# Performance work log

Measured on AMD Instinct MI355X. Metric: run time of the kernel, lower is better.

## Reference

```python
import jax, jax.numpy as jnp
import numpy as np

SCALE = 1.0


def _chamfer_pair(a, b):
    # a: [N,3], b: [M,3] -> (dist1 [N], dist2 [M]) squared NN distances
    # ||a-b||^2 = ||a||^2 + ||b||^2 - 2 a.b
    aa = jnp.sum(a * a, axis=-1)            # [N]
    bb = jnp.sum(b * b, axis=-1)            # [M]
    ab = jnp.einsum('nd,md->nm', a, b)      # [N,M]
    d = aa[:, None] + bb[None, :] - 2.0 * ab
    d = jnp.maximum(d, 0.0)
    return jnp.min(d, axis=1), jnp.min(d, axis=0)


def reference(p1, p2):
    # p1, p2: [B, N, 3]; scale applied before distance, matching the torch module
    a = p1 * SCALE
    b = p2 * SCALE
    dist1, dist2 = jax.vmap(_chamfer_pair)(a, b)  # [B,N], [B,M]
    # per-sample loss = mean(dist1) + mean(dist2); total averaged over batch
    per_sample = jnp.mean(dist1, axis=1) + jnp.mean(dist2, axis=1)  # [B]
    return jnp.mean(per_sample).reshape(1)


def setup_inputs() -> dict:
    key = jax.random.key(0)
    k1, k2 = jax.random.split(key)
    B, N, M = 4, 8192, 8192
    p1 = jax.random.normal(k1, (B, N, 3), dtype=jnp.float32)
    p2 = jax.random.normal(k2, (B, M, 3), dtype=jnp.float32)
    return {"p1": p1, "p2": p2}
```

## Files before the change

kernel.cpp:

```cpp
#include <hip/hip_runtime.h>
#include <math.h>

#define BATCH   4
#define NPTS    8192
#define THREADS 256
#define QPT     4
#define QPB     (THREADS * QPT)
#define QTILES  (NPTS / QPB)

static constexpr float SCALE = 1.0f;


template<int TCH>
__global__ __launch_bounds__(THREADS, 8)
void chamfer_min_kernel(const float* __restrict__ p1,
                        const float* __restrict__ p2,
                        float* __restrict__ pm)
{
    constexpr int CHUNK = NPTS / TCH;
    __shared__ float4 lds4[CHUNK];

    const int bid = blockIdx.x;
    const int c   = bid % TCH;
    const int qt  = (bid / TCH) % QTILES;
    const int b   = (bid / (TCH * QTILES)) % BATCH;
    const int dir = bid / (TCH * QTILES * BATCH);

    const float* qptr = (dir == 0 ? p1 : p2) + (size_t)b * NPTS * 3;
    const float* tptr = (dir == 0 ? p2 : p1) + (size_t)b * NPTS * 3;

    const float* tsrc = tptr + (size_t)c * CHUNK * 3;
    for (int i = threadIdx.x; i < CHUNK; i += THREADS) {
        const float x = tsrc[3 * i + 0] * SCALE;
        const float y = tsrc[3 * i + 1] * SCALE;
        const float z = tsrc[3 * i + 2] * SCALE;
        const float bb = fmaf(z, z, fmaf(y, y, x * x));
        lds4[i] = make_float4(-2.0f * x, -2.0f * y, -2.0f * z, bb);
    }

    const int t  = threadIdx.x;
    const int q0 = qt * QPB + t;
    float qx[QPT], qy[QPT], qz[QPT], qmin[QPT];
    #pragma unroll
    for (int k = 0; k < QPT; ++k) {
        const int q = q0 + k * THREADS;
        qx[k] = qptr[q * 3 + 0] * SCALE;
        qy[k] = qptr[q * 3 + 1] * SCALE;
        qz[k] = qptr[q * 3 + 2] * SCALE;
        qmin[k] = 3.0e38f;
    }

    __syncthreads();

    for (int j = 0; j < CHUNK; j += 8) {
        #pragma unroll
        for (int i = 0; i < 8; i += 2) {
            const float4 t0 = lds4[j + i];
            const float4 t1 = lds4[j + i + 1];
            #pragma unroll
            for (int k = 0; k < QPT; ++k) {
                float s0 = fmaf(qx[k], t0.x, t0.w);
                s0 = fmaf(qy[k], t0.y, s0);
                s0 = fmaf(qz[k], t0.z, s0);
                float s1 = fmaf(qx[k], t1.x, t1.w);
                s1 = fmaf(qy[k], t1.y, s1);
                s1 = fmaf(qz[k], t1.z, s1);
                qmin[k] = fminf(qmin[k], fminf(s0, s1));
            }
        }
    }

    #pragma unroll
    for (int k = 0; k < QPT; ++k) {
        const float aa = fmaf(qz[k], qz[k], fmaf(qy[k], qy[k], qx[k] * qx[k]));
        const int q = q0 + k * THREADS;
        pm[((size_t)(dir * BATCH + b) * NPTS + q) * TCH + c] = qmin[k] + aa;
    }
}

template<int TCH>
__global__ __launch_bounds__(512)
void chamfer_reduce_kernel(const float* __restrict__ pm,
                           float* __restrict__ bsum)
{
    const int idx = blockIdx.x * 512 + threadIdx.x;
    const float4* p4 = reinterpret_cast<const float4*>(pm + (size_t)idx * TCH);
    float m = 3.0e38f;
    #pragma unroll
    for (int i = 0; i < TCH / 4; ++i) {
        const float4 u = p4[i];
        m = fminf(m, fminf(fminf(u.x, u.y), fminf(u.z, u.w)));
    }
    m = fmaxf(m, 0.0f);

    #pragma unroll
    for (int o = 32; o > 0; o >>= 1) m += __shfl_down(m, o, 64);

    __shared__ float red[8];
    const int wave = threadIdx.x >> 6;
    const int lane = threadIdx.x & 63;
    if (lane == 0) red[wave] = m;
    __syncthreads();
    if (threadIdx.x == 0) {
        float s = 0.0f;
        #pragma unroll
        for (int w = 0; w < 8; ++w) s += red[w];
        bsum[blockIdx.x] = s;
    }
}

__global__ __launch_bounds__(64)
void chamfer_final_kernel(const float* __restrict__ bsum,
                          float* __restrict__ out)
{
    const int t = threadIdx.x;
    float s0 = bsum[t];
    float s1 = bsum[64 + t];
    #pragma unroll
    for (int o = 32; o > 0; o >>= 1) {
        s0 += __shfl_down(s0, o, 64);
        s1 += __shfl_down(s1, o, 64);
    }
    if (t == 0) {
        out[0] = s0 / (float)(BATCH * NPTS) + s1 / (float)(BATCH * NPTS);
    }
}

template<int TCH>
static void launch_all(const float* p1, const float* p2, float* out,
                       void* d_ws, hipStream_t stream)
{
    float* pm   = (float*)d_ws;
    float* bsum = pm + (size_t)2 * BATCH * NPTS * TCH;

    chamfer_min_kernel<TCH><<<2 * BATCH * QTILES * TCH, THREADS, 0, stream>>>(p1, p2, pm);
    chamfer_reduce_kernel<TCH><<<128, 512, 0, stream>>>(pm, bsum);
    chamfer_final_kernel<<<1, 64, 0, stream>>>(bsum, out);
}

extern "C" void kernel_launch(void* const* d_in, const int* in_sizes, int n_in,
                              void* d_out, int out_size, void* d_ws, size_t ws_size,
                              hipStream_t stream) {
    const float* p1 = (const float*)d_in[0];
    const float* p2 = (const float*)d_in[1];
    float* out = (float*)d_out;

    const size_t need32 = (size_t)2 * BATCH * NPTS * 32 * sizeof(float) + 512;
    if (ws_size >= need32) {
        launch_all<32>(p1, p2, out, d_ws, stream);
    } else {
        launch_all<8>(p1, p2, out, d_ws, stream);
    }
}
```

Baseline: 105.1 us.

## Raise target chunking and queries per thread, fuse final reduction via atomics

The default configuration moves from 32 target chunks with 4 queries per thread to 64 chunks with 8 queries per thread. This doubles query register reuse per shared-memory load and keeps enough blocks in the grid. The partial-min buffer becomes chunk-major so reduce threads read coalesced data. The separate final kernel is dropped: reduce blocks atomically accumulate into two sums, and a last-block ticket writes the output, saving one launch. The risks are higher register pressure at 8 queries per thread and float atomic ordering nondeterminism.

```diff
diff --git a/kernel.cpp b/kernel.cpp
--- a/kernel.cpp
+++ b/kernel.cpp
@@ -4,20 +4,24 @@
 #define BATCH   4
 #define NPTS    8192
 #define THREADS 256
-#define QPT     4
-#define QPB     (THREADS * QPT)
-#define QTILES  (NPTS / QPB)
+#define NQ      (2 * BATCH * NPTS)
 
 static constexpr float SCALE = 1.0f;
 
 
-template<int TCH>
+template<int TCH, int QPT>
 __global__ __launch_bounds__(THREADS, 8)
 void chamfer_min_kernel(const float* __restrict__ p1,
                         const float* __restrict__ p2,
-                        float* __restrict__ pm)
+                        float* __restrict__ pm,
+                        float* __restrict__ acc)
 {
-    constexpr int CHUNK = NPTS / TCH;
+    constexpr int CHUNK  = NPTS / TCH;
+    constexpr int QPB    = THREADS * QPT;
+    constexpr int QTILES = NPTS / QPB;
+
+    if (blockIdx.x == 0 && threadIdx.x < 3) acc[threadIdx.x] = 0.0f;
+
     __shared__ float4 lds4[CHUNK];
 
     const int bid = blockIdx.x;
@@ -74,23 +78,21 @@
     for (int k = 0; k < QPT; ++k) {
         const float aa = fmaf(qz[k], qz[k], fmaf(qy[k], qy[k], qx[k] * qx[k]));
         const int q = q0 + k * THREADS;
-        pm[((size_t)(dir * BATCH + b) * NPTS + q) * TCH + c] = qmin[k] + aa;
+        pm[(size_t)c * NQ + (size_t)(dir * BATCH + b) * NPTS + q] = qmin[k] + aa;
     }
 }
 
 template<int TCH>
 __global__ __launch_bounds__(512)
 void chamfer_reduce_kernel(const float* __restrict__ pm,
-                           float* __restrict__ bsum)
+                           float* __restrict__ acc,
+                           float* __restrict__ out)
 {
     const int idx = blockIdx.x * 512 + threadIdx.x;
-    const float4* p4 = reinterpret_cast<const float4*>(pm + (size_t)idx * TCH);
     float m = 3.0e38f;
     #pragma unroll
-    for (int i = 0; i < TCH / 4; ++i) {
-        const float4 u = p4[i];
-        m = fminf(m, fminf(fminf(u.x, u.y), fminf(u.z, u.w)));
-    }
+    for (int c = 0; c < TCH; ++c)
+        m = fminf(m, pm[(size_t)c * NQ + idx]);
     m = fmaxf(m, 0.0f);
 
     #pragma unroll
@@ -105,37 +107,28 @@
         float s = 0.0f;
         #pragma unroll
         for (int w = 0; w < 8; ++w) s += red[w];
-        bsum[blockIdx.x] = s;
+        atomicAdd(&acc[blockIdx.x >> 6], s);
+        __threadfence();
+        const unsigned tk = atomicAdd(reinterpret_cast<unsigned*>(acc + 2), 1u);
+        if (tk == 127) {
+            __threadfence();
+            const float s0 = atomicAdd(&acc[0], 0.0f);
+            const float s1 = atomicAdd(&acc[1], 0.0f);
+            out[0] = (s0 + s1) * (1.0f / (float)(BATCH * NPTS));
+        }
     }
 }
 
-__global__ __launch_bounds__(64)
-void chamfer_final_kernel(const float* __restrict__ bsum,
-                          float* __restrict__ out)
-{
-    const int t = threadIdx.x;
-    float s0 = bsum[t];
-    float s1 = bsum[64 + t];
-    #pragma unroll
-    for (int o = 32; o > 0; o >>= 1) {
-        s0 += __shfl_down(s0, o, 64);
-        s1 += __shfl_down(s1, o, 64);
-    }
-    if (t == 0) {
-        out[0] = s0 / (float)(BATCH * NPTS) + s1 / (float)(BATCH * NPTS);
-    }
-}
-
-template<int TCH>
+template<int TCH, int QPT>
 static void launch_all(const float* p1, const float* p2, float* out,
                        void* d_ws, hipStream_t stream)
 {
-    float* pm   = (float*)d_ws;
-    float* bsum = pm + (size_t)2 * BATCH * NPTS * TCH;
+    constexpr int QTILES = NPTS / (THREADS * QPT);
+    float* pm  = (float*)d_ws;
+    float* acc = pm + (size_t)TCH * NQ;
 
-    chamfer_min_kernel<TCH><<<2 * BATCH * QTILES * TCH, THREADS, 0, stream>>>(p1, p2, pm);
-    chamfer_reduce_kernel<TCH><<<128, 512, 0, stream>>>(pm, bsum);
-    chamfer_final_kernel<<<1, 64, 0, stream>>>(bsum, out);
+    chamfer_min_kernel<TCH, QPT><<<2 * BATCH * QTILES * TCH, THREADS, 0, stream>>>(p1, p2, pm, acc);
+    chamfer_reduce_kernel<TCH><<<128, 512, 0, stream>>>(pm, acc, out);
 }
 
 extern "C" void kernel_launch(void* const* d_in, const int* in_sizes, int n_in,
@@ -145,10 +138,10 @@
     const float* p2 = (const float*)d_in[1];
     float* out = (float*)d_out;
 
-    const size_t need32 = (size_t)2 * BATCH * NPTS * 32 * sizeof(float) + 512;
-    if (ws_size >= need32) {
-        launch_all<32>(p1, p2, out, d_ws, stream);
+    const size_t need64 = (size_t)64 * NQ * sizeof(float) + 64;
+    if (ws_size >= need64) {
+        launch_all<64, 8>(p1, p2, out, d_ws, stream);
     } else {
-        launch_all<8>(p1, p2, out, d_ws, stream);
+        launch_all<32, 4>(p1, p2, out, d_ws, stream);
     }
 }
```

Result: slower. 107.3 us (+2.1%).
